# Kernel optimization log

Measured on AMD Instinct MI355X. Metric: run time of the kernel, lower is better.

The kernel has to match this reference:

```python
import jax, jax.numpy as jnp
import numpy as np

SEQ_LEN, HORIZON = 12, 12
B, N, DIN, DOUT, U = 16, 512, 2, 1, 64
NEG = -1e9


def _gat(x, W, a, b, mask):
    # x: (B, N, F_in); W: (F_in, G); a: (2, G); mask: (N, N) bool
    h = jnp.einsum('bnf,fg->bng', x, W)            # (B, N, G)
    src = jnp.einsum('bng,g->bn', h, a[0])         # (B, N)
    dst = jnp.einsum('bng,g->bn', h, a[1])         # (B, N)
    e = jax.nn.leaky_relu(src[:, :, None] + dst[:, None, :], 0.2)  # (B, N, N)
    e = jnp.where(mask[None], e, NEG)
    alpha = jax.nn.softmax(e, axis=-1)
    return jnp.einsum('bij,bjg->big', alpha, h) + b


def _cell(x, h_prev, W_ru, a_ru, b_ru, W_c, a_c, b_c, mask):
    # graph-attention GRU cell: x (B,N,Din), h_prev (B,N,U)
    xh = jnp.concatenate([x, h_prev], axis=-1)
    ru = jax.nn.sigmoid(_gat(xh, W_ru, a_ru, b_ru, mask))   # (B,N,2U)
    r, u = jnp.split(ru, 2, axis=-1)
    xc = jnp.concatenate([x, r * h_prev], axis=-1)
    c = jnp.tanh(_gat(xc, W_c, a_c, b_c, mask))
    return u * h_prev + (1.0 - u) * c


def setup_inputs() -> dict:
    key = jax.random.key(0)
    ks = jax.random.split(key, 16)
    s = 0.05
    inp = {
        'inputs': jax.random.normal(ks[0], (SEQ_LEN, B, N * DIN), jnp.float32),
        'adj': jax.random.uniform(ks[1], (N, N), jnp.float32),
        # encoder GAGRU cell (input_dim = DIN)
        'enc_W_ru': jax.random.normal(ks[2], (DIN + U, 2 * U), jnp.float32) * s,
        'enc_a_ru': jax.random.normal(ks[3], (2, 2 * U), jnp.float32) * s,
        'enc_b_ru': jnp.zeros((2 * U,), jnp.float32),
        'enc_W_c': jax.random.normal(ks[4], (DIN + U, U), jnp.float32) * s,
        'enc_a_c': jax.random.normal(ks[5], (2, U), jnp.float32) * s,
        'enc_b_c': jnp.zeros((U,), jnp.float32),
        # decoder GAGRU cell (input_dim = DOUT)
        'dec_W_ru': jax.random.normal(ks[6], (DOUT + U, 2 * U), jnp.float32) * s,
        'dec_a_ru': jax.random.normal(ks[7], (2, 2 * U), jnp.float32) * s,
        'dec_b_ru': jnp.zeros((2 * U,), jnp.float32),
        'dec_W_c': jax.random.normal(ks[8], (DOUT + U, U), jnp.float32) * s,
        'dec_a_c': jax.random.normal(ks[9], (2, U), jnp.float32) * s,
        'dec_b_c': jnp.zeros((U,), jnp.float32),
        # projection Linear(rnn_units -> output_dim)
        'proj_W': jax.random.normal(ks[10], (U, DOUT), jnp.float32) * s,
        'proj_b': jnp.zeros((DOUT,), jnp.float32),
    }
    return inp


def reference(inputs, adj, enc_W_ru, enc_a_ru, enc_b_ru, enc_W_c, enc_a_c, enc_b_c,
              dec_W_ru, dec_a_ru, dec_b_ru, dec_W_c, dec_a_c, dec_b_c, proj_W, proj_b):
    mask = (adj > 0.9) | jnp.eye(N, dtype=bool)
    x_seq = inputs.reshape(SEQ_LEN, B, N, DIN)

    # ---- encoder: scan GAGRU cell over seq_len ----
    def enc_step(h, x_t):
        h_new = _cell(x_t, h, enc_W_ru, enc_a_ru, enc_b_ru, enc_W_c, enc_a_c, enc_b_c, mask)
        return h_new, None

    h0 = jnp.zeros((B, N, U), inputs.dtype)
    h_enc, _ = jax.lax.scan(enc_step, h0, x_seq)

    def dec_step(carry, _):
        y_prev, h = carry
        h_new = _cell(y_prev, h, dec_W_ru, dec_a_ru, dec_b_ru, dec_W_c, dec_a_c, dec_b_c, mask)
        y = jnp.einsum('bnu,ud->bnd', h_new, proj_W) + proj_b  # (B, N, DOUT)
        return (y, h_new), y

    go = jnp.zeros((B, N, DOUT), inputs.dtype)
    _, outputs = jax.lax.scan(dec_step, (go, h_enc), None, length=HORIZON)
    return outputs  # (horizon, B, N, DOUT)
```

## Files before the change

### kernel.cpp

```cpp
#include <hip/hip_runtime.h>
#include <math.h>


#define NB 16
#define NN 512
#define NU 64
#define CAP 128
#define WPB 8

#define AS1 __attribute__((address_space(1)))
#define AS3 __attribute__((address_space(3)))

__device__ __forceinline__ void ld_lds16(float* lds_uniform, const float* g_perlane) {
#if __has_builtin(__builtin_amdgcn_global_load_lds)
  __builtin_amdgcn_global_load_lds((const AS1 unsigned int*)g_perlane,
                                   (AS3 unsigned int*)lds_uniform, 16, 0, 0);
#else
  int lane = threadIdx.x & 63;
  *(float4*)(lds_uniform + lane * 4) = *(const float4*)(g_perlane);
#endif
}

__device__ __forceinline__ void stage_weights(float* sW, const float* W, int TB,
                                              int w, int lane) {
  for (int c = w; c * 1024 < TB; c += WPB) {
    int off = c * 1024 + lane * 16;
    if (off < TB)
      ld_lds16((float*)((char*)sW + c * 1024), (const float*)((const char*)W + off));
  }
}

__device__ __forceinline__ float rlane(float v, int l) {
  return __int_as_float(__builtin_amdgcn_readlane(__float_as_int(v), l));
}
__device__ __forceinline__ int rlane_i(int v, int l) {
  return __builtin_amdgcn_readlane(v, l);
}
__device__ __forceinline__ float wave_max(float v) {
  #pragma unroll
  for (int s = 1; s < 64; s <<= 1) v = fmaxf(v, __shfl_xor(v, s));
  return v;
}
__device__ __forceinline__ float wave_sum(float v) {
  #pragma unroll
  for (int s = 1; s < 64; s <<= 1) v += __shfl_xor(v, s);
  return v;
}
__device__ __forceinline__ void wave_sum2(float& x, float& y) {
  #pragma unroll
  for (int s = 1; s < 64; s <<= 1) { x += __shfl_xor(x, s); y += __shfl_xor(y, s); }
}
__device__ __forceinline__ float fast_rcp(float x) {
#if __has_builtin(__builtin_amdgcn_rcpf)
  return __builtin_amdgcn_rcpf(x);
#else
  return 1.0f / x;
#endif
}
__device__ __forceinline__ float sigmoid_f(float x) {
  return fast_rcp(1.0f + __expf(-x));
}
__device__ __forceinline__ float tanh_f(float x) {
  return 1.0f - 2.0f * fast_rcp(__expf(2.0f * x) + 1.0f);
}

__device__ __forceinline__ void decode_block(int bx, int w, int& b, int& i) {
  int x = bx & 7, k = bx >> 3;
  b = (x << 1) | (k >> 6);
  i = ((k & 63) << 3) | w;
}

__global__ __launch_bounds__(64) void k_adj(const float* __restrict__ adj,
                                            int* __restrict__ cnt,
                                            int* __restrict__ idx) {
  int i = blockIdx.x;
  int l = threadIdx.x;
  int base = 0;
  #pragma unroll
  for (int c = 0; c < 8; ++c) {
    int j = c * 64 + l;
    bool pred = (adj[i * NN + j] > 0.9f) || (j == i);
    unsigned long long m = __ballot(pred);
    int pos = base + __popcll(m & ((1ull << l) - 1ull));
    if (pred && pos < CAP) idx[i * CAP + pos] = j;
    base += __popcll(m);
  }
  int total = base > CAP ? CAP : base;
  for (int p = total + l; p < CAP; p += 64) idx[i * CAP + p] = i;
  if (l == 0) cnt[i] = total;
}

template <int DIN>
__global__ __launch_bounds__(512, 6) void k_phaseB(
    const int* __restrict__ cnt, const int* __restrict__ idx,
    const float* __restrict__ h_ru, const float* __restrict__ src_ru,
    const float* __restrict__ dst_ru, const float* __restrict__ b_ru,
    const float* __restrict__ h, const float* __restrict__ x_ptr,
    const float* __restrict__ W_c, const float* __restrict__ a_c,
    float* __restrict__ h_c, float* __restrict__ src_c,
    float* __restrict__ dst_c, float* __restrict__ u_buf) {
  constexpr int TB = (DIN + NU) * NU * 4;
  __shared__ float sW[(DIN + NU) * NU];
  __shared__ float sh[WPB * NU];
  const int tid = threadIdx.x;
  const int w = tid >> 6, lane = tid & 63;

  stage_weights(sW, W_c, TB, w, lane);

  int b, i;
  decode_block(blockIdx.x, w, b, i);
  const int base_bi = (b << 9) + i;
  const float* __restrict__ hrb = h_ru + ((size_t)b << 16);
  const float* __restrict__ drb = dst_ru + (b << 9);

  const int c_ = cnt[i];
  const float si = src_ru[base_bi];
  const int j0 = idx[(i << 7) + lane];
  const int j1 = idx[(i << 7) + 64 + lane];
  float e0 = -1e30f, e1 = -1e30f;
  if (lane < c_)      { float t = si + drb[j0]; e0 = t >= 0.f ? t : 0.2f * t; }
  if (lane + 64 < c_) { float t = si + drb[j1]; e1 = t >= 0.f ? t : 0.2f * t; }
  float m = wave_max(fmaxf(e0, e1));
  float p0 = (lane < c_) ? __expf(e0 - m) : 0.f;
  float p1 = (lane + 64 < c_) ? __expf(e1 - m) : 0.f;
  float inv = fast_rcp(wave_sum(p0 + p1));
  p0 *= inv; p1 *= inv;

  const int g0 = lane << 1;
  float A0 = 0.f, A1 = 0.f, B0 = 0.f, B1 = 0.f;
  const int cc = (c_ + 15) & ~15;
  for (int base = 0; base < cc; base += 16) {
    float2 hv[16];
    #pragma unroll
    for (int q = 0; q < 16; ++q) {
      int jj = base + q;
      int sl = jj & 63;
      int j = (jj < 64) ? rlane_i(j0, sl) : rlane_i(j1, sl);
      hv[q] = *(const float2*)(hrb + (j << 7) + g0);
    }
    #pragma unroll
    for (int q = 0; q < 16; ++q) {
      int jj = base + q;
      int sl = jj & 63;
      float pv = (jj < 64) ? rlane(p0, sl) : rlane(p1, sl);
      if (q & 1) { B0 = fmaf(pv, hv[q].x, B0); B1 = fmaf(pv, hv[q].y, B1); }
      else       { A0 = fmaf(pv, hv[q].x, A0); A1 = fmaf(pv, hv[q].y, A1); }
    }
  }
  A0 += B0; A1 += B1;

  const float2 br = *(const float2*)(b_ru + g0);
  const float ru0 = sigmoid_f(A0 + br.x);
  const float ru1 = sigmoid_f(A1 + br.y);

  if (lane < 32) {
    float2 hh = *(const float2*)(h + ((size_t)base_bi << 6) + g0);
    *(float2*)&sh[(w << 6) + g0] = make_float2(ru0 * hh.x, ru1 * hh.y);
  } else {
    *(float2*)(u_buf + ((size_t)base_bi << 6) + (g0 - 64)) = make_float2(ru0, ru1);
  }

  __syncthreads();

  float acc;
  if (DIN == 2) {
    float2 xv = *(const float2*)(x_ptr + ((size_t)base_bi << 1));
    acc = xv.x * sW[lane];
    acc = fmaf(xv.y, sW[NU + lane], acc);
  } else {
    acc = x_ptr[base_bi] * sW[lane];
  }
  const float* __restrict__ sWh = sW + DIN * NU;
  const float* shw = sh + (w << 6);
  #pragma unroll
  for (int f2 = 0; f2 < 32; ++f2) {
    float2 rv = *(const float2*)(shw + 2 * f2);
    acc = fmaf(rv.x, sWh[(2 * f2) * NU + lane], acc);
    acc = fmaf(rv.y, sWh[(2 * f2 + 1) * NU + lane], acc);
  }
  h_c[((size_t)base_bi << 6) + lane] = acc;
  float s0 = acc * a_c[lane];
  float s1 = acc * a_c[NU + lane];
  wave_sum2(s0, s1);
  if (lane == 0) { src_c[base_bi] = s0; dst_c[base_bi] = s1; }
}

template <int UPD, int DIN_NEXT, int XMODE, int OUT>
__global__ __launch_bounds__(512, 6) void k_phaseA(
    const int* __restrict__ cnt, const int* __restrict__ idx,
    const float* __restrict__ h_c, const float* __restrict__ src_c,
    const float* __restrict__ dst_c, const float* __restrict__ b_c,
    const float* __restrict__ u_buf, float* __restrict__ h,
    const float* __restrict__ proj_W, const float* __restrict__ proj_b,
    float* __restrict__ out_slice, float* __restrict__ y_buf,
    const float* __restrict__ x_ptr,
    const float* __restrict__ W_ru, const float* __restrict__ a_ru,
    float* __restrict__ h_ru, float* __restrict__ src_ru,
    float* __restrict__ dst_ru) {
  constexpr int SWN = (DIN_NEXT > 0) ? (DIN_NEXT + NU) * 128 : 1;
  constexpr int TB = (DIN_NEXT > 0) ? SWN * 4 : 0;
  __shared__ float sW[SWN];
  __shared__ float sh[WPB * NU];
  const int tid = threadIdx.x;
  const int w = tid >> 6, lane = tid & 63;

  if (DIN_NEXT > 0) stage_weights(sW, W_ru, TB, w, lane);

  int b, i;
  decode_block(blockIdx.x, w, b, i);
  const int base_bi = (b << 9) + i;

  float hn = 0.f;
  if (UPD) {
    const float* __restrict__ hcb = h_c + ((size_t)b << 15);
    const float* __restrict__ dcb = dst_c + (b << 9);
    const int c_ = cnt[i];
    const float si = src_c[base_bi];
    const int j0 = idx[(i << 7) + lane];
    const int j1 = idx[(i << 7) + 64 + lane];
    float e0 = -1e30f, e1 = -1e30f;
    if (lane < c_)      { float t = si + dcb[j0]; e0 = t >= 0.f ? t : 0.2f * t; }
    if (lane + 64 < c_) { float t = si + dcb[j1]; e1 = t >= 0.f ? t : 0.2f * t; }
    float m = wave_max(fmaxf(e0, e1));
    float p0 = (lane < c_) ? __expf(e0 - m) : 0.f;
    float p1 = (lane + 64 < c_) ? __expf(e1 - m) : 0.f;
    float inv = fast_rcp(wave_sum(p0 + p1));
    p0 *= inv; p1 *= inv;

    float A = 0.f, Bacc = 0.f;
    const int cc = (c_ + 15) & ~15;
    for (int base = 0; base < cc; base += 16) {
      float hv[16];
      #pragma unroll
      for (int q = 0; q < 16; ++q) {
        int jj = base + q;
        int sl = jj & 63;
        int j = (jj < 64) ? rlane_i(j0, sl) : rlane_i(j1, sl);
        hv[q] = hcb[(j << 6) + lane];
      }
      #pragma unroll
      for (int q = 0; q < 16; ++q) {
        int jj = base + q;
        int sl = jj & 63;
        float pv = (jj < 64) ? rlane(p0, sl) : rlane(p1, sl);
        if (q & 1) Bacc = fmaf(pv, hv[q], Bacc);
        else       A = fmaf(pv, hv[q], A);
      }
    }
    A += Bacc;
    const float cc_ = tanh_f(A + b_c[lane]);
    const float u = u_buf[((size_t)base_bi << 6) + lane];
    const float ho = h[((size_t)base_bi << 6) + lane];
    hn = fmaf(u, ho - cc_, cc_);
  }
  h[((size_t)base_bi << 6) + lane] = hn;
  sh[(w << 6) + lane] = hn;

  float y = 0.f;
  if (OUT) {
    float t = wave_sum(hn * proj_W[lane]);
    y = t + proj_b[0];
    if (lane == 0) { out_slice[base_bi] = y; y_buf[base_bi] = y; }
  }

  if (DIN_NEXT > 0) {
    __syncthreads();
    const int g0 = lane << 1;
    float a0, a1;
    if (XMODE == 0) {
      if (DIN_NEXT == 2) {
        float2 xv = *(const float2*)(x_ptr + ((size_t)base_bi << 1));
        a0 = xv.x * sW[g0];
        a1 = xv.x * sW[g0 + 1];
        a0 = fmaf(xv.y, sW[128 + g0], a0);
        a1 = fmaf(xv.y, sW[128 + g0 + 1], a1);
      } else {
        float xv = x_ptr[base_bi];
        a0 = xv * sW[g0]; a1 = xv * sW[g0 + 1];
      }
    } else if (XMODE == 2) {
      a0 = y * sW[g0]; a1 = y * sW[g0 + 1];
    } else {
      a0 = 0.f; a1 = 0.f;
    }
    const float* __restrict__ sWh = sW + DIN_NEXT * 128;
    const float* shw = sh + (w << 6);
    #pragma unroll
    for (int f2 = 0; f2 < 32; ++f2) {
      float2 hp = *(const float2*)(shw + 2 * f2);
      float2 w0 = *(const float2*)(sWh + (2 * f2) * 128 + g0);
      float2 w1 = *(const float2*)(sWh + (2 * f2 + 1) * 128 + g0);
      a0 = fmaf(hp.x, w0.x, a0); a1 = fmaf(hp.x, w0.y, a1);
      a0 = fmaf(hp.y, w1.x, a0); a1 = fmaf(hp.y, w1.y, a1);
    }
    *(float2*)(h_ru + ((size_t)base_bi << 7) + g0) = make_float2(a0, a1);
    const float2 ar0 = *(const float2*)(a_ru + g0);
    const float2 ar1 = *(const float2*)(a_ru + 128 + g0);
    float s0 = a0 * ar0.x + a1 * ar0.y;
    float s1 = a0 * ar1.x + a1 * ar1.y;
    wave_sum2(s0, s1);
    if (lane == 0) { src_ru[base_bi] = s0; dst_ru[base_bi] = s1; }
  }
}

extern "C" void kernel_launch(void* const* d_in, const int* in_sizes, int n_in,
                              void* d_out, int out_size, void* d_ws, size_t ws_size,
                              hipStream_t stream) {
  (void)in_sizes; (void)n_in; (void)out_size; (void)ws_size;
  const float* inputs   = (const float*)d_in[0];
  const float* adj      = (const float*)d_in[1];
  const float* enc_W_ru = (const float*)d_in[2];
  const float* enc_a_ru = (const float*)d_in[3];
  const float* enc_b_ru = (const float*)d_in[4];
  const float* enc_W_c  = (const float*)d_in[5];
  const float* enc_a_c  = (const float*)d_in[6];
  const float* enc_b_c  = (const float*)d_in[7];
  const float* dec_W_ru = (const float*)d_in[8];
  const float* dec_a_ru = (const float*)d_in[9];
  const float* dec_b_ru = (const float*)d_in[10];
  const float* dec_W_c  = (const float*)d_in[11];
  const float* dec_a_c  = (const float*)d_in[12];
  const float* dec_b_c  = (const float*)d_in[13];
  const float* proj_W   = (const float*)d_in[14];
  const float* proj_b   = (const float*)d_in[15];
  float* out = (float*)d_out;

  char* ws = (char*)d_ws;
  int*   cnt    = (int*)ws;
  int*   idx    = (int*)(ws + 2048);
  float* h      = (float*)(ws + 264192);
  float* h_ru   = (float*)(ws + 2361344);
  float* src_ru = (float*)(ws + 6555648);
  float* dst_ru = (float*)(ws + 6588416);
  float* h_c    = (float*)(ws + 6621184);
  float* src_c  = (float*)(ws + 8718336);
  float* dst_c  = (float*)(ws + 8751104);
  float* u_buf  = (float*)(ws + 8783872);
  float* y_buf  = (float*)(ws + 10881024);

  hipMemsetAsync(y_buf, 0, NB * NN * sizeof(float), stream);
  k_adj<<<NN, 64, 0, stream>>>(adj, cnt, idx);

  const int GRID = (NB * NN) / WPB;

  k_phaseA<0, 2, 0, 0><<<GRID, 512, 0, stream>>>(cnt, idx, h_c, src_c, dst_c,
      enc_b_c, u_buf, h, proj_W, proj_b, nullptr, y_buf,
      inputs, enc_W_ru, enc_a_ru, h_ru, src_ru, dst_ru);

  for (int t = 0; t < 12; ++t) {
    k_phaseB<2><<<GRID, 512, 0, stream>>>(cnt, idx, h_ru, src_ru, dst_ru, enc_b_ru,
        h, inputs + (size_t)t * NB * NN * 2, enc_W_c, enc_a_c,
        h_c, src_c, dst_c, u_buf);
    if (t < 11)
      k_phaseA<1, 2, 0, 0><<<GRID, 512, 0, stream>>>(cnt, idx, h_c, src_c, dst_c,
          enc_b_c, u_buf, h, proj_W, proj_b, nullptr, y_buf,
          inputs + (size_t)(t + 1) * NB * NN * 2, enc_W_ru, enc_a_ru,
          h_ru, src_ru, dst_ru);
    else
      k_phaseA<1, 1, 1, 0><<<GRID, 512, 0, stream>>>(cnt, idx, h_c, src_c, dst_c,
          enc_b_c, u_buf, h, proj_W, proj_b, nullptr, y_buf,
          nullptr, dec_W_ru, dec_a_ru, h_ru, src_ru, dst_ru);
  }

  for (int k = 0; k < 12; ++k) {
    k_phaseB<1><<<GRID, 512, 0, stream>>>(cnt, idx, h_ru, src_ru, dst_ru, dec_b_ru,
        h, y_buf, dec_W_c, dec_a_c, h_c, src_c, dst_c, u_buf);
    if (k < 11)
      k_phaseA<1, 1, 2, 1><<<GRID, 512, 0, stream>>>(cnt, idx, h_c, src_c, dst_c,
          dec_b_c, u_buf, h, proj_W, proj_b, out + (size_t)k * NB * NN, y_buf,
          nullptr, dec_W_ru, dec_a_ru, h_ru, src_ru, dst_ru);
    else
      k_phaseA<1, 0, 1, 1><<<GRID, 512, 0, stream>>>(cnt, idx, h_c, src_c, dst_c,
          dec_b_c, u_buf, h, proj_W, proj_b, out + (size_t)k * NB * NN, y_buf,
          nullptr, dec_W_ru, dec_a_ru, h_ru, src_ru, dst_ru);
  }
}
```

Before: 801.7 us.

## Split batch into two halves run concurrently on two streams

Splits the batch into two independent halves of eight sequences each and runs the full encoder/decoder kernel chain for each half on its own stream, with fork and join events. The aim is to overlap one half's launch gaps and tail under-utilisation with the other half's work, since batches are independent. Each grid is halved, so a single kernel fills fewer CUs, and the block decode now maps eight consecutive blocks to eight batches within the half. It relies on both streams sharing the workspace buffers without overlapping writes, which holds because the halves index disjoint batch ranges.

Result: faster. 758.6 us (-5.4%).

```diff
diff --git a/kernel.cpp b/kernel.cpp
--- a/kernel.cpp
+++ b/kernel.cpp
@@ -64,10 +64,10 @@
   return 1.0f - 2.0f * fast_rcp(__expf(2.0f * x) + 1.0f);
 }
 
-__device__ __forceinline__ void decode_block(int bx, int w, int& b, int& i) {
-  int x = bx & 7, k = bx >> 3;
-  b = (x << 1) | (k >> 6);
-  i = ((k & 63) << 3) | w;
+__device__ __forceinline__ void decode_half(int bx, int w, int bhalf,
+                                            int& b, int& i) {
+  b = bhalf + (bx & 7);
+  i = (((bx >> 3)) << 3) | w;
 }
 
 __global__ __launch_bounds__(64) void k_adj(const float* __restrict__ adj,
@@ -98,7 +98,7 @@
     const float* __restrict__ h, const float* __restrict__ x_ptr,
     const float* __restrict__ W_c, const float* __restrict__ a_c,
     float* __restrict__ h_c, float* __restrict__ src_c,
-    float* __restrict__ dst_c, float* __restrict__ u_buf) {
+    float* __restrict__ dst_c, float* __restrict__ u_buf, int bhalf) {
   constexpr int TB = (DIN + NU) * NU * 4;
   __shared__ float sW[(DIN + NU) * NU];
   __shared__ float sh[WPB * NU];
@@ -108,7 +108,7 @@
   stage_weights(sW, W_c, TB, w, lane);
 
   int b, i;
-  decode_block(blockIdx.x, w, b, i);
+  decode_half(blockIdx.x, w, bhalf, b, i);
   const int base_bi = (b << 9) + i;
   const float* __restrict__ hrb = h_ru + ((size_t)b << 16);
   const float* __restrict__ drb = dst_ru + (b << 9);
@@ -196,7 +196,7 @@
     const float* __restrict__ x_ptr,
     const float* __restrict__ W_ru, const float* __restrict__ a_ru,
     float* __restrict__ h_ru, float* __restrict__ src_ru,
-    float* __restrict__ dst_ru) {
+    float* __restrict__ dst_ru, int bhalf) {
   constexpr int SWN = (DIN_NEXT > 0) ? (DIN_NEXT + NU) * 128 : 1;
   constexpr int TB = (DIN_NEXT > 0) ? SWN * 4 : 0;
   __shared__ float sW[SWN];
@@ -207,7 +207,7 @@
   if (DIN_NEXT > 0) stage_weights(sW, W_ru, TB, w, lane);
 
   int b, i;
-  decode_block(blockIdx.x, w, b, i);
+  decode_half(blockIdx.x, w, bhalf, b, i);
   const int base_bi = (b << 9) + i;
 
   float hn = 0.f;
@@ -338,40 +338,59 @@
   float* u_buf  = (float*)(ws + 8783872);
   float* y_buf  = (float*)(ws + 10881024);
 
+  static hipStream_t s2 = nullptr;
+  static hipEvent_t evFork = nullptr, evJoin = nullptr;
+  if (s2 == nullptr) {
+    hipStreamCreateWithFlags(&s2, hipStreamNonBlocking);
+    hipEventCreateWithFlags(&evFork, hipEventDisableTiming);
+    hipEventCreateWithFlags(&evJoin, hipEventDisableTiming);
+  }
+
   hipMemsetAsync(y_buf, 0, NB * NN * sizeof(float), stream);
   k_adj<<<NN, 64, 0, stream>>>(adj, cnt, idx);
 
-  const int GRID = (NB * NN) / WPB;
-
-  k_phaseA<0, 2, 0, 0><<<GRID, 512, 0, stream>>>(cnt, idx, h_c, src_c, dst_c,
-      enc_b_c, u_buf, h, proj_W, proj_b, nullptr, y_buf,
-      inputs, enc_W_ru, enc_a_ru, h_ru, src_ru, dst_ru);
-
-  for (int t = 0; t < 12; ++t) {
-    k_phaseB<2><<<GRID, 512, 0, stream>>>(cnt, idx, h_ru, src_ru, dst_ru, enc_b_ru,
-        h, inputs + (size_t)t * NB * NN * 2, enc_W_c, enc_a_c,
-        h_c, src_c, dst_c, u_buf);
-    if (t < 11)
-      k_phaseA<1, 2, 0, 0><<<GRID, 512, 0, stream>>>(cnt, idx, h_c, src_c, dst_c,
-          enc_b_c, u_buf, h, proj_W, proj_b, nullptr, y_buf,
-          inputs + (size_t)(t + 1) * NB * NN * 2, enc_W_ru, enc_a_ru,
-          h_ru, src_ru, dst_ru);
-    else
-      k_phaseA<1, 1, 1, 0><<<GRID, 512, 0, stream>>>(cnt, idx, h_c, src_c, dst_c,
-          enc_b_c, u_buf, h, proj_W, proj_b, nullptr, y_buf,
-          nullptr, dec_W_ru, dec_a_ru, h_ru, src_ru, dst_ru);
-  }
-
-  for (int k = 0; k < 12; ++k) {
-    k_phaseB<1><<<GRID, 512, 0, stream>>>(cnt, idx, h_ru, src_ru, dst_ru, dec_b_ru,
-        h, y_buf, dec_W_c, dec_a_c, h_c, src_c, dst_c, u_buf);
-    if (k < 11)
-      k_phaseA<1, 1, 2, 1><<<GRID, 512, 0, stream>>>(cnt, idx, h_c, src_c, dst_c,
-          dec_b_c, u_buf, h, proj_W, proj_b, out + (size_t)k * NB * NN, y_buf,
-          nullptr, dec_W_ru, dec_a_ru, h_ru, src_ru, dst_ru);
-    else
-      k_phaseA<1, 0, 1, 1><<<GRID, 512, 0, stream>>>(cnt, idx, h_c, src_c, dst_c,
-          dec_b_c, u_buf, h, proj_W, proj_b, out + (size_t)k * NB * NN, y_buf,
-          nullptr, dec_W_ru, dec_a_ru, h_ru, src_ru, dst_ru);
-  }
-}
+  hipEventRecord(evFork, stream);
+  hipStreamWaitEvent(s2, evFork, 0);
+
+  const int GRID = (NB * NN) / (2 * WPB);
+
+  for (int half = 0; half < 2; ++half) {
+    hipStream_t st = (half == 0) ? stream : s2;
+    const int bh = half * 8;
+
+    k_phaseA<0, 2, 0, 0><<<GRID, 512, 0, st>>>(cnt, idx, h_c, src_c, dst_c,
+        enc_b_c, u_buf, h, proj_W, proj_b, nullptr, y_buf,
+        inputs, enc_W_ru, enc_a_ru, h_ru, src_ru, dst_ru, bh);
+
+    for (int t = 0; t < 12; ++t) {
+      k_phaseB<2><<<GRID, 512, 0, st>>>(cnt, idx, h_ru, src_ru, dst_ru, enc_b_ru,
+          h, inputs + (size_t)t * NB * NN * 2, enc_W_c, enc_a_c,
+          h_c, src_c, dst_c, u_buf, bh);
+      if (t < 11)
+        k_phaseA<1, 2, 0, 0><<<GRID, 512, 0, st>>>(cnt, idx, h_c, src_c, dst_c,
+            enc_b_c, u_buf, h, proj_W, proj_b, nullptr, y_buf,
+            inputs + (size_t)(t + 1) * NB * NN * 2, enc_W_ru, enc_a_ru,
+            h_ru, src_ru, dst_ru, bh);
+      else
+        k_phaseA<1, 1, 1, 0><<<GRID, 512, 0, st>>>(cnt, idx, h_c, src_c, dst_c,
+            enc_b_c, u_buf, h, proj_W, proj_b, nullptr, y_buf,
+            nullptr, dec_W_ru, dec_a_ru, h_ru, src_ru, dst_ru, bh);
+    }
+
+    for (int k = 0; k < 12; ++k) {
+      k_phaseB<1><<<GRID, 512, 0, st>>>(cnt, idx, h_ru, src_ru, dst_ru, dec_b_ru,
+          h, y_buf, dec_W_c, dec_a_c, h_c, src_c, dst_c, u_buf, bh);
+      if (k < 11)
+        k_phaseA<1, 1, 2, 1><<<GRID, 512, 0, st>>>(cnt, idx, h_c, src_c, dst_c,
+            dec_b_c, u_buf, h, proj_W, proj_b, out + (size_t)k * NB * NN, y_buf,
+            nullptr, dec_W_ru, dec_a_ru, h_ru, src_ru, dst_ru, bh);
+      else
+        k_phaseA<1, 0, 1, 1><<<GRID, 512, 0, st>>>(cnt, idx, h_c, src_c, dst_c,
+            dec_b_c, u_buf, h, proj_W, proj_b, out + (size_t)k * NB * NN, y_buf,
+            nullptr, dec_W_ru, dec_a_ru, h_ru, src_ru, dst_ru, bh);
+    }
+  }
+
+  hipEventRecord(evJoin, s2);
+  hipStreamWaitEvent(stream, evJoin, 0);
+}
```
